# Kernel tuning notes

Measured on AMD Instinct MI355X. Metric: run time of the kernel, lower is better.

## Reference

```python
import jax, jax.numpy as jnp
import numpy as np

B, S, D, A = 8, 4096, 128, 128


def _pos_encoding(seq_len, dim):
    # sin/cos positional encoding, same construction as the torch buffer
    pos = np.arange(seq_len, dtype=np.float32)[:, None]
    div = np.exp(np.arange(0, dim, 2, dtype=np.float32) * (-np.log(10000.0) / dim))
    pe = np.zeros((seq_len, dim), dtype=np.float32)
    pe[:, 0::2] = np.sin(pos * div)
    pe[:, 1::2] = np.cos(pos * div)
    return jnp.asarray(pe)


def setup_inputs() -> dict:
    key = jax.random.key(0)
    ks = jax.random.split(key, 7)
    sc = 1.0 / np.sqrt(D)
    return {
        "x": jax.random.normal(ks[0], (B, S, D), dtype=jnp.float32),
        "Wq": jax.random.normal(ks[1], (D, A), dtype=jnp.float32) * sc,
        "bq": jnp.zeros((A,), dtype=jnp.float32),
        "Wk": jax.random.normal(ks[2], (D, A), dtype=jnp.float32) * sc,
        "bk": jnp.zeros((A,), dtype=jnp.float32),
        "Wv": jax.random.normal(ks[3], (D, A), dtype=jnp.float32) * sc,
        "bv": jnp.zeros((A,), dtype=jnp.float32),
    }


def reference(x, Wq, bq, Wk, bk, Wv, bv):
    b, s, d = x.shape
    pe = _pos_encoding(s, d)  # [S, D]
    xp = x + pe[None]  # broadcast add of positional encoding
    q = xp @ Wq + bq  # [B, S, A]
    k = xp @ Wk + bk
    v = xp @ Wv + bv
    scale = 1.0 / jnp.sqrt(jnp.asarray(Wq.shape[1], dtype=jnp.float32))
    scores = jnp.einsum("bsa,bta->bst", q, k) * scale  # [B, S, S]
    weights = jax.nn.softmax(scores, axis=-1)
    out = jnp.einsum("bst,bta->bsa", weights, v)  # [B, S, A]
    return out
```

## Files before the change

kernel.cpp:

```cpp
#include <hip/hip_runtime.h>

#define BB 8
#define SS 4096
#define DD 128

typedef __attribute__((ext_vector_type(8))) short v8s;
typedef __attribute__((ext_vector_type(4))) short v4s;
typedef __attribute__((ext_vector_type(4))) float v4f;
typedef __attribute__((ext_vector_type(16))) float v16f;

__device__ __forceinline__ unsigned short f2bf(float f) {
    unsigned int u = __float_as_uint(f);
    u += 0x7fffu + ((u >> 16) & 1u);
    return (unsigned short)(u >> 16);
}
__device__ __forceinline__ unsigned int pk_bf16(float a, float b) {
    unsigned int ua = __float_as_uint(a) + 0x8000u;
    unsigned int ub = __float_as_uint(b) + 0x8000u;
    return __builtin_amdgcn_perm(ub, ua, 0x07060302u);
}

#if !defined(__HIP_DEVICE_COMPILE__)
#define MFMA16(a, b, c) (c)
#define MFMA32(a, b, c) (c)
#else
#define MFMA16(a, b, c) __builtin_amdgcn_mfma_f32_16x16x32_bf16((a), (b), (c), 0, 0, 0)
#define MFMA32(a, b, c) __builtin_amdgcn_mfma_f32_32x32x16_bf16((a), (b), (c), 0, 0, 0)
#endif

#if !defined(__HIP_DEVICE_COMPILE__)
#define EXP2F(x) exp2f(x)
#elif __has_builtin(__builtin_amdgcn_exp2f)
#define EXP2F(x) __builtin_amdgcn_exp2f(x)
#else
#define EXP2F(x) exp2f(x)
#endif

#define QSCALE 0.12751743f
#define FIXM 24.0f

__global__ __launch_bounds__(256) void prep_kernel(
    const float* __restrict__ Wq, const float* __restrict__ Wk,
    const float* __restrict__ Wv, unsigned short* __restrict__ Wt,
    float* __restrict__ pe)
{
    int bid = blockIdx.x;
    int tid = threadIdx.x;
    if (bid < 192) {
        int id = bid * 256 + tid;
        int w = id >> 14;
        int n = (id >> 7) & 127;
        int k = id & 127;
        const float* W = (w == 0) ? Wq : (w == 1) ? Wk : Wv;
        Wt[id] = f2bf(W[k * 128 + n]);
    } else {
        int id = (bid - 192) * 256 + tid;
        int s = id >> 5;
        int d0 = (id & 31) * 4;
        v4f r;
#pragma unroll
        for (int j = 0; j < 4; j += 2) {
            float freq = __expf((float)(d0 + j) * -0.07195578415606394f);
            float arg = (float)s * freq;
            r[j] = __sinf(arg);
            r[j + 1] = __cosf(arg);
        }
        *(v4f*)(pe + (size_t)s * DD + d0) = r;
    }
}

__global__ __launch_bounds__(256, 3) void proj_kernel(
    const float* __restrict__ x, const float* __restrict__ pe,
    const unsigned short* __restrict__ Wt,
    const float* __restrict__ bq, const float* __restrict__ bk,
    const float* __restrict__ bv,
    unsigned short* __restrict__ qo, unsigned short* __restrict__ ko,
    unsigned short* __restrict__ vo)
{
    __shared__ __attribute__((aligned(16))) unsigned short w_lds[128 * 136];
    __shared__ __attribute__((aligned(16))) unsigned short o_lds[9216];

    const int tid = threadIdx.x;
    const int wave = tid >> 6;
    const int lane = tid & 63;
    const int quad = lane >> 4;
    const int l15 = lane & 15;
    const int bid = blockIdx.x;
    const int mat = bid % 3;
    const int rbase = (bid / 3) * 64;

    const unsigned short* Wp = Wt + (mat << 14);
#pragma unroll
    for (int it = 0; it < 8; ++it) {
        int id = it * 256 + tid;
        int n = id >> 4, c8 = id & 15;
        *(v8s*)(w_lds + n * 136 + c8 * 8) = *(const v8s*)(Wp + n * 128 + c8 * 8);
    }

    const int flatrow = rbase + wave * 16 + l15;
    const int srow = flatrow & 4095;
    v8s af[4];
#pragma unroll
    for (int kc = 0; kc < 4; ++kc) {
        const int kbase = kc * 32 + quad * 8;
        const v4f* xp = (const v4f*)(x + (size_t)flatrow * DD + kbase);
        const v4f* pp = (const v4f*)(pe + (size_t)srow * DD + kbase);
        v4f x0 = xp[0], x1 = xp[1], p0 = pp[0], p1 = pp[1];
        v8s a;
#pragma unroll
        for (int j = 0; j < 4; ++j) a[j] = (short)f2bf(x0[j] + p0[j]);
#pragma unroll
        for (int j = 0; j < 4; ++j) a[4 + j] = (short)f2bf(x1[j] + p1[j]);
        af[kc] = a;
    }

    const float* bias = (mat == 0) ? bq : (mat == 1) ? bk : bv;
    __syncthreads();

#pragma unroll
    for (int nb = 0; nb < 8; ++nb) {
        const int col = nb * 16 + l15;
        v4f acc = {0.f, 0.f, 0.f, 0.f};
#pragma unroll
        for (int kc = 0; kc < 4; ++kc) {
            v8s bf = *(const v8s*)(w_lds + col * 136 + kc * 32 + quad * 8);
            acc = MFMA16(af[kc], bf, acc);
        }
        float bval = bias[col];
#pragma unroll
        for (int reg = 0; reg < 4; ++reg) {
            int lr = wave * 16 + quad * 4 + reg;
            float val = acc[reg] + bval;
            if (mat == 0) {
                o_lds[lr * 136 + col] = f2bf(val * QSCALE);
            } else if (mat == 1) {
                o_lds[lr * 136 + col] = f2bf(val);
            } else {
                o_lds[col * 72 + lr] = f2bf(val);
            }
        }
    }
    __syncthreads();

    if (mat <= 1) {
        unsigned short* outp = (mat == 0) ? qo : ko;
#pragma unroll
        for (int it = 0; it < 4; ++it) {
            int id = it * 256 + tid;
            int r = id >> 4, c8 = id & 15;
            *(v8s*)(outp + (size_t)(rbase + r) * DD + c8 * 8) =
                *(const v8s*)(o_lds + r * 136 + c8 * 8);
        }
    } else {
        const int b0 = rbase >> 12, s0 = rbase & 4095;
#pragma unroll
        for (int it = 0; it < 4; ++it) {
            int id = it * 256 + tid;
            int a = id >> 3, c = id & 7;
            *(v8s*)(vo + ((size_t)(b0 * 128 + a)) * SS + s0 + c * 8) =
                *(const v8s*)(o_lds + a * 72 + c * 8);
        }
    }
}

#define KT 32
#define HKEYS 2048
#define NT (HKEYS / KT)
__global__ __launch_bounds__(512, 2) void flash_kernel(
    const unsigned short* __restrict__ qg,
    const unsigned short* __restrict__ kg,
    const unsigned short* __restrict__ vg,
    float* __restrict__ out)
{
    __shared__ __attribute__((aligned(16))) unsigned short k_lds[2][2][4096];
    __shared__ __attribute__((aligned(16))) unsigned short v_lds[2][2][4096];
    __shared__ float xl[128];

    const int tid = threadIdx.x;
    const int wave = tid >> 6;
    const int lane = tid & 63;
    const int hi = lane >> 5;
    const int l31 = lane & 31;
    const int half = tid >> 8;
    const int qs = wave & 3;
    const int bid = blockIdx.x;
    const int b = bid & 7;
    const int qt = bid >> 3;
    const int qbase = qt * 128;

    const size_t qrow = (size_t)(b * SS + qbase + qs * 32 + l31) * DD;
    v8s qf[8];
#pragma unroll
    for (int kc = 0; kc < 8; ++kc)
        qf[kc] = *(const v8s*)(qg + qrow + kc * 16 + hi * 8);

    v16f o[4];
#pragma unroll
    for (int fg = 0; fg < 4; ++fg)
#pragma unroll
        for (int r = 0; r < 16; ++r) o[fg][r] = 0.f;
    v16f lacc;
#pragma unroll
    for (int r = 0; r < 16; ++r) lacc[r] = 0.f;

    v8s ones;
#pragma unroll
    for (int j = 0; j < 8; ++j) ones[j] = (short)0x3F80;

    const unsigned short* kb = kg + (size_t)b * SS * DD + (size_t)half * HKEYS * DD;
    const unsigned short* vb = vg + (size_t)b * DD * SS + half * HKEYS;

    const int tid2 = tid & 255;
    const int kr_r = tid2 >> 4, kr_c = tid2 & 15;
    const int va = tid2 >> 2, vc8 = tid2 & 3;
    v8s kr[2], vr[2];

    auto load_tile = [&](int t) {
        const unsigned short* kp = kb + (size_t)t * KT * DD;
        const unsigned short* vp = vb + t * KT;
#pragma unroll
        for (int it = 0; it < 2; ++it) {
            kr[it] = *(const v8s*)(kp + (size_t)(kr_r + it * 16) * DD + kr_c * 8);
            vr[it] = *(const v8s*)(vp + (size_t)(va + it * 64) * SS + vc8 * 8);
        }
    };
    auto store_tile = [&](int p) {
#pragma unroll
        for (int it = 0; it < 2; ++it) {
            int r = kr_r + it * 16;
            *(v8s*)(&k_lds[half][p][r * 128 + ((kr_c ^ (r & 7)) << 3)]) = kr[it];
            int a = va + it * 64;
            v4s lo = {vr[it][0], vr[it][1], vr[it][2], vr[it][3]};
            v4s hv = {vr[it][4], vr[it][5], vr[it][6], vr[it][7]};
            int cc = vc8 >> 1, h = vc8 & 1;
            int sw = (a & 3) ^ ((a >> 2) & 1);
            *(v4s*)(&v_lds[half][p][a * 32 + (((cc ^ sw) << 3) + h * 4)]) = lo;
            *(v4s*)(&v_lds[half][p][a * 32 + ((((cc + 2) ^ sw) << 3) + h * 4)]) = hv;
        }
    };
    auto compute = [&](int p) {
        v16f s;
#pragma unroll
        for (int r = 0; r < 16; ++r) s[r] = -FIXM;
#pragma unroll
        for (int kc = 0; kc < 8; ++kc) {
            v8s af = *(const v8s*)(&k_lds[half][p][l31 * 128 +
                                   (((kc * 2 + hi) ^ (l31 & 7)) << 3)]);
            s = MFMA32(af, qf[kc], s);
        }
        float e[16];
#pragma unroll
        for (int r = 0; r < 16; ++r) e[r] = EXP2F(s[r]);
        union { v8s v[2]; unsigned int u[8]; } P;
#pragma unroll
        for (int g = 0; g < 2; ++g)
#pragma unroll
            for (int m = 0; m < 4; ++m)
                P.u[g * 4 + m] = pk_bf16(e[2 * m + 8 * g], e[2 * m + 8 * g + 1]);
#pragma unroll
        for (int g = 0; g < 2; ++g) {
            lacc = MFMA32(P.v[g], ones, lacc);
#pragma unroll
            for (int fg = 0; fg < 4; ++fg) {
                int row = fg * 32 + l31;
                int sw = (row & 3) ^ ((row >> 2) & 1);
                v8s bf = *(const v8s*)(&v_lds[half][p][row * 32 +
                                       (((2 * hi + g) ^ sw) << 3)]);
                o[fg] = MFMA32(P.v[g], bf, o[fg]);
            }
        }
    };

    load_tile(0);
    store_tile(0);
    load_tile(1);
    __syncthreads();
#pragma unroll 1
    for (int kt = 0; kt < NT; kt += 2) {
        store_tile(1);
        if (kt + 2 < NT) load_tile(kt + 2);
        compute(0);
        __syncthreads();
        if (kt + 2 < NT) {
            store_tile(0);
            if (kt + 3 < NT) load_tile(kt + 3);
        }
        compute(1);
        __syncthreads();
    }

    float* kf = (float*)&k_lds[0][0][0];
    float* vf = (float*)&v_lds[0][0][0];
    float* xch = (qs < 2) ? (kf + qs * 4096) : (vf + (qs - 2) * 4096);

    if (half == 1) {
#pragma unroll
        for (int fg = 0; fg < 4; ++fg) {
            v4f* base = (v4f*)(xch + fg * 1024 + lane * 16);
#pragma unroll
            for (int c = 0; c < 4; ++c) {
                v4f t = {o[fg][c * 4 + 0], o[fg][c * 4 + 1],
                         o[fg][c * 4 + 2], o[fg][c * 4 + 3]};
                base[c ^ (lane & 3)] = t;
            }
        }
        if (l31 == 0) {
#pragma unroll
            for (int r = 0; r < 16; ++r) {
                int qr = (r & 3) + 8 * (r >> 2) + 4 * hi;
                xl[qs * 32 + qr] = lacc[r];
            }
        }
    }
    __syncthreads();
    if (half == 0) {
#pragma unroll
        for (int fg = 0; fg < 4; ++fg) {
            const v4f* base = (const v4f*)(xch + fg * 1024 + lane * 16);
#pragma unroll
            for (int c = 0; c < 4; ++c) {
                v4f t = base[c ^ (lane & 3)];
#pragma unroll
                for (int j = 0; j < 4; ++j) o[fg][c * 4 + j] += t[j];
            }
        }
        float ir[16];
#pragma unroll
        for (int r = 0; r < 16; ++r) {
            int qr = (r & 3) + 8 * (r >> 2) + 4 * hi;
            ir[r] = 1.0f / (lacc[r] + xl[qs * 32 + qr]);
        }
#pragma unroll
        for (int fg = 0; fg < 4; ++fg)
#pragma unroll
            for (int r = 0; r < 16; ++r) {
                int qr = (r & 3) + 8 * (r >> 2) + 4 * hi;
                out[(size_t)(b * SS + qbase + qs * 32 + qr) * DD + fg * 32 + l31] =
                    o[fg][r] * ir[r];
            }
    }
}

extern "C" void kernel_launch(void* const* d_in, const int* in_sizes, int n_in,
                              void* d_out, int out_size, void* d_ws, size_t ws_size,
                              hipStream_t stream)
{
    const float* x  = (const float*)d_in[0];
    const float* Wq = (const float*)d_in[1];
    const float* bq = (const float*)d_in[2];
    const float* Wk = (const float*)d_in[3];
    const float* bk = (const float*)d_in[4];
    const float* Wv = (const float*)d_in[5];
    const float* bv = (const float*)d_in[6];
    float* out = (float*)d_out;

    unsigned short* Wt = (unsigned short*)d_ws;
    unsigned short* q  = Wt + 49152;
    unsigned short* k  = q + (size_t)BB * SS * DD;
    unsigned short* vT = k + (size_t)BB * SS * DD;
    float* pe = (float*)(vT + (size_t)BB * SS * DD);

    hipLaunchKernelGGL(prep_kernel, dim3(704), dim3(256), 0, stream,
                       Wq, Wk, Wv, Wt, pe);
    hipLaunchKernelGGL(proj_kernel, dim3(BB * SS / 64 * 3), dim3(256), 0, stream,
                       x, pe, Wt, bq, bk, bv, q, k, vT);
    hipLaunchKernelGGL(flash_kernel, dim3(BB * SS / 128), dim3(512), 0, stream,
                       q, k, vT, out);
}
```

Measured before the change: 179.0 us.

## Restructure flash kernel: direct global-to-LDS loads, 4-way key split, 64-row waves

The attention kernel now stages K/V tiles with global_load_lds straight into LDS instead of going through registers, synchronised with explicit vmcnt/lgkmcnt waits and raw barriers. Keys are split four ways across wave pairs, with each wave handling 64 query rows (two MFMA accumulator sets), so each K/V LDS fragment read is reused twice. Row sums are now taken with VALU adds instead of an MFMA against a ones vector, and the fixed -24 offset is dropped. The cost is a three-step LDS reduction of partial outputs and higher register pressure. The V layout in the prep kernel is permuted to match the new LDS swizzle.

```diff
diff --git a/kernel.cpp b/kernel.cpp
--- a/kernel.cpp
+++ b/kernel.cpp
@@ -5,7 +5,6 @@
 #define DD 128
 
 typedef __attribute__((ext_vector_type(8))) short v8s;
-typedef __attribute__((ext_vector_type(4))) short v4s;
 typedef __attribute__((ext_vector_type(4))) float v4f;
 typedef __attribute__((ext_vector_type(16))) float v16f;
 
@@ -23,9 +22,26 @@
 #if !defined(__HIP_DEVICE_COMPILE__)
 #define MFMA16(a, b, c) (c)
 #define MFMA32(a, b, c) (c)
+#define GLDS16(g, l)
+#define WAITVM(n)
+#define WAITLGKM()
+#define BAR()
 #else
 #define MFMA16(a, b, c) __builtin_amdgcn_mfma_f32_16x16x32_bf16((a), (b), (c), 0, 0, 0)
 #define MFMA32(a, b, c) __builtin_amdgcn_mfma_f32_32x32x16_bf16((a), (b), (c), 0, 0, 0)
+#define GLDS16(g, l)                                                         \
+    __builtin_amdgcn_global_load_lds(                                        \
+        (const __attribute__((address_space(1))) unsigned int*)(g),          \
+        (__attribute__((address_space(3))) unsigned int*)(l), 16, 0, 0)
+#define WAITVM(n) asm volatile("s_waitcnt vmcnt(" #n ")" ::: "memory")
+#define WAITLGKM() asm volatile("s_waitcnt lgkmcnt(0)" ::: "memory")
+#define BAR()                                                                \
+    do {                                                                     \
+        asm volatile("" ::: "memory");                                       \
+        __builtin_amdgcn_s_barrier();                                        \
+        __builtin_amdgcn_sched_barrier(0);                                   \
+        asm volatile("" ::: "memory");                                       \
+    } while (0)
 #endif
 
 #if !defined(__HIP_DEVICE_COMPILE__)
@@ -37,7 +53,6 @@
 #endif
 
 #define QSCALE 0.12751743f
-#define FIXM 24.0f
 
 __global__ __launch_bounds__(256) void prep_kernel(
     const float* __restrict__ Wq, const float* __restrict__ Wk,
@@ -115,6 +130,7 @@
     }
 
     const float* bias = (mat == 0) ? bq : (mat == 1) ? bk : bv;
+    const int quadp = ((quad & 1) << 1) | (quad >> 1);
     __syncthreads();
 
 #pragma unroll
@@ -129,14 +145,16 @@
         float bval = bias[col];
 #pragma unroll
         for (int reg = 0; reg < 4; ++reg) {
-            int lr = wave * 16 + quad * 4 + reg;
             float val = acc[reg] + bval;
             if (mat == 0) {
+                int lr = wave * 16 + quad * 4 + reg;
                 o_lds[lr * 136 + col] = f2bf(val * QSCALE);
             } else if (mat == 1) {
+                int lr = wave * 16 + quad * 4 + reg;
                 o_lds[lr * 136 + col] = f2bf(val);
             } else {
-                o_lds[col * 72 + lr] = f2bf(val);
+                int plr = wave * 16 + quadp * 4 + reg;
+                o_lds[col * 72 + plr] = f2bf(val);
             }
         }
     }
@@ -164,180 +182,203 @@
 }
 
 #define KT 32
-#define HKEYS 2048
-#define NT (HKEYS / KT)
+#define QKEYS 1024
+#define NT2 (QKEYS / KT)
 __global__ __launch_bounds__(512, 2) void flash_kernel(
-    const unsigned short* __restrict__ qg,
-    const unsigned short* __restrict__ kg,
-    const unsigned short* __restrict__ vg,
-    float* __restrict__ out)
+    const unsigned short* __restrict__ qp,
+    const unsigned short* __restrict__ kp,
+    const unsigned short* __restrict__ vp,
+    float* __restrict__ outp)
 {
-    __shared__ __attribute__((aligned(16))) unsigned short k_lds[2][2][4096];
-    __shared__ __attribute__((aligned(16))) unsigned short v_lds[2][2][4096];
-    __shared__ float xl[128];
+    __shared__ __attribute__((aligned(16))) unsigned short k_lds[4][2][4096];
+    __shared__ __attribute__((aligned(16))) unsigned short v_lds[4][2][4096];
+    __shared__ float xl[8][64];
 
     const int tid = threadIdx.x;
     const int wave = tid >> 6;
     const int lane = tid & 63;
     const int hi = lane >> 5;
     const int l31 = lane & 31;
-    const int half = tid >> 8;
-    const int qs = wave & 3;
+    const int qtr = wave >> 1;
+    const int w = wave & 1;
+    const int qs = wave & 1;
     const int bid = blockIdx.x;
     const int b = bid & 7;
     const int qt = bid >> 3;
     const int qbase = qt * 128;
 
-    const size_t qrow = (size_t)(b * SS + qbase + qs * 32 + l31) * DD;
-    v8s qf[8];
-#pragma unroll
-    for (int kc = 0; kc < 8; ++kc)
-        qf[kc] = *(const v8s*)(qg + qrow + kc * 16 + hi * 8);
-
-    v16f o[4];
+    const size_t qrow0 = (size_t)(b * SS + qbase + qs * 64 + l31) * DD;
+    v8s qf0[8], qf1[8];
+#pragma unroll
+    for (int kc = 0; kc < 8; ++kc) {
+        qf0[kc] = *(const v8s*)(qp + qrow0 + kc * 16 + hi * 8);
+        qf1[kc] = *(const v8s*)(qp + qrow0 + (size_t)32 * DD + kc * 16 + hi * 8);
+    }
+
+    v16f o0[4], o1[4];
 #pragma unroll
     for (int fg = 0; fg < 4; ++fg)
 #pragma unroll
-        for (int r = 0; r < 16; ++r) o[fg][r] = 0.f;
-    v16f lacc;
-#pragma unroll
-    for (int r = 0; r < 16; ++r) lacc[r] = 0.f;
-
-    v8s ones;
-#pragma unroll
-    for (int j = 0; j < 8; ++j) ones[j] = (short)0x3F80;
-
-    const unsigned short* kb = kg + (size_t)b * SS * DD + (size_t)half * HKEYS * DD;
-    const unsigned short* vb = vg + (size_t)b * DD * SS + half * HKEYS;
-
-    const int tid2 = tid & 255;
-    const int kr_r = tid2 >> 4, kr_c = tid2 & 15;
-    const int va = tid2 >> 2, vc8 = tid2 & 3;
-    v8s kr[2], vr[2];
-
-    auto load_tile = [&](int t) {
-        const unsigned short* kp = kb + (size_t)t * KT * DD;
-        const unsigned short* vp = vb + t * KT;
-#pragma unroll
-        for (int it = 0; it < 2; ++it) {
-            kr[it] = *(const v8s*)(kp + (size_t)(kr_r + it * 16) * DD + kr_c * 8);
-            vr[it] = *(const v8s*)(vp + (size_t)(va + it * 64) * SS + vc8 * 8);
-        }
+        for (int r = 0; r < 16; ++r) { o0[fg][r] = 0.f; o1[fg][r] = 0.f; }
+    float lp0 = 0.f, lp1 = 0.f;
+
+    const int koff = qtr * 16384 + l31 * 256 + ((hi << 4) ^ ((l31 & 7) << 4));
+    const int hx3 = (hi << 4) ^ ((l31 & 3) << 4);
+    const int vaddr0 = qtr * 16384 + l31 * 64 + hx3;
+    const int vaddr1 = qtr * 16384 + l31 * 64 + (hx3 ^ 32);
+
+    const int krw = lane >> 4, ksl = lane & 15;
+    const int e_sh = krw * 128 + ((ksl ^ krw) << 3);
+    const unsigned short* kq =
+        kp + ((size_t)(b * SS) + qtr * QKEYS) * DD + w * 2048;
+    const unsigned short* kp0_ = kq + e_sh;
+    const unsigned short* kp4_ = kq + (e_sh ^ 32);
+    const int vrw = lane >> 2, vsl = lane & 3;
+    const int e_v = vrw * 4096 + ((vsl ^ (vrw & 3)) << 3);
+    const unsigned short* vq =
+        vp + (size_t)b * DD * SS + qtr * QKEYS + (size_t)w * 262144 + e_v;
+
+    auto stage = [&](int p, int t) {
+        unsigned short* kd = &k_lds[qtr][p][w * 2048];
+        unsigned short* vd = &v_lds[qtr][p][w * 2048];
+        const unsigned short* ks0 = kp0_ + (size_t)t * 4096;
+        const unsigned short* ks4 = kp4_ + (size_t)t * 4096;
+        const unsigned short* vs = vq + (size_t)t * 32;
+        GLDS16(ks0, kd);
+        GLDS16(ks4 + 512, kd + 512);
+        GLDS16(ks0 + 1024, kd + 1024);
+        GLDS16(ks4 + 1536, kd + 1536);
+        GLDS16(vs, vd);
+        GLDS16(vs + 65536, vd + 512);
+        GLDS16(vs + 131072, vd + 1024);
+        GLDS16(vs + 196608, vd + 1536);
     };
-    auto store_tile = [&](int p) {
-#pragma unroll
-        for (int it = 0; it < 2; ++it) {
-            int r = kr_r + it * 16;
-            *(v8s*)(&k_lds[half][p][r * 128 + ((kr_c ^ (r & 7)) << 3)]) = kr[it];
-            int a = va + it * 64;
-            v4s lo = {vr[it][0], vr[it][1], vr[it][2], vr[it][3]};
-            v4s hv = {vr[it][4], vr[it][5], vr[it][6], vr[it][7]};
-            int cc = vc8 >> 1, h = vc8 & 1;
-            int sw = (a & 3) ^ ((a >> 2) & 1);
-            *(v4s*)(&v_lds[half][p][a * 32 + (((cc ^ sw) << 3) + h * 4)]) = lo;
-            *(v4s*)(&v_lds[half][p][a * 32 + ((((cc + 2) ^ sw) << 3) + h * 4)]) = hv;
+
+    auto compute = [&](int p) {
+        v16f s0, s1;
+#pragma unroll
+        for (int r = 0; r < 16; ++r) { s0[r] = 0.f; s1[r] = 0.f; }
+#pragma unroll
+        for (int kc = 0; kc < 8; ++kc) {
+            v8s af = *(const v8s*)((const char*)k_lds +
+                                   ((koff ^ (kc << 5)) + p * 8192));
+            s0 = MFMA32(af, qf0[kc], s0);
+            s1 = MFMA32(af, qf1[kc], s1);
+        }
+        union PU { v8s v[2]; unsigned int u[8]; } P0, P1;
+        float e[16];
+#pragma unroll
+        for (int r = 0; r < 16; ++r) e[r] = EXP2F(s0[r]);
+        lp0 += (((e[0] + e[1]) + (e[2] + e[3])) + ((e[4] + e[5]) + (e[6] + e[7]))) +
+               (((e[8] + e[9]) + (e[10] + e[11])) + ((e[12] + e[13]) + (e[14] + e[15])));
+#pragma unroll
+        for (int g = 0; g < 2; ++g)
+#pragma unroll
+            for (int m = 0; m < 4; ++m)
+                P0.u[g * 4 + m] = pk_bf16(e[2 * m + 8 * g], e[2 * m + 8 * g + 1]);
+#pragma unroll
+        for (int r = 0; r < 16; ++r) e[r] = EXP2F(s1[r]);
+        lp1 += (((e[0] + e[1]) + (e[2] + e[3])) + ((e[4] + e[5]) + (e[6] + e[7]))) +
+               (((e[8] + e[9]) + (e[10] + e[11])) + ((e[12] + e[13]) + (e[14] + e[15])));
+#pragma unroll
+        for (int g = 0; g < 2; ++g)
+#pragma unroll
+            for (int m = 0; m < 4; ++m)
+                P1.u[g * 4 + m] = pk_bf16(e[2 * m + 8 * g], e[2 * m + 8 * g + 1]);
+#pragma unroll
+        for (int g = 0; g < 2; ++g) {
+            const int va = g ? vaddr1 : vaddr0;
+#pragma unroll
+            for (int fg = 0; fg < 4; ++fg) {
+                v8s bf = *(const v8s*)((const char*)v_lds +
+                                       (va + fg * 2048 + p * 8192));
+                o0[fg] = MFMA32(P0.v[g], bf, o0[fg]);
+                o1[fg] = MFMA32(P1.v[g], bf, o1[fg]);
+            }
         }
     };
-    auto compute = [&](int p) {
-        v16f s;
-#pragma unroll
-        for (int r = 0; r < 16; ++r) s[r] = -FIXM;
-#pragma unroll
-        for (int kc = 0; kc < 8; ++kc) {
-            v8s af = *(const v8s*)(&k_lds[half][p][l31 * 128 +
-                                   (((kc * 2 + hi) ^ (l31 & 7)) << 3)]);
-            s = MFMA32(af, qf[kc], s);
-        }
-        float e[16];
-#pragma unroll
-        for (int r = 0; r < 16; ++r) e[r] = EXP2F(s[r]);
-        union { v8s v[2]; unsigned int u[8]; } P;
-#pragma unroll
-        for (int g = 0; g < 2; ++g)
-#pragma unroll
-            for (int m = 0; m < 4; ++m)
-                P.u[g * 4 + m] = pk_bf16(e[2 * m + 8 * g], e[2 * m + 8 * g + 1]);
-#pragma unroll
-        for (int g = 0; g < 2; ++g) {
-            lacc = MFMA32(P.v[g], ones, lacc);
-#pragma unroll
-            for (int fg = 0; fg < 4; ++fg) {
-                int row = fg * 32 + l31;
-                int sw = (row & 3) ^ ((row >> 2) & 1);
-                v8s bf = *(const v8s*)(&v_lds[half][p][row * 32 +
-                                       (((2 * hi + g) ^ sw) << 3)]);
-                o[fg] = MFMA32(P.v[g], bf, o[fg]);
-            }
-        }
-    };
-
-    load_tile(0);
-    store_tile(0);
-    load_tile(1);
-    __syncthreads();
+
+    stage(0, 0);
 #pragma unroll 1
-    for (int kt = 0; kt < NT; kt += 2) {
-        store_tile(1);
-        if (kt + 2 < NT) load_tile(kt + 2);
+    for (int t = 0; t < NT2; t += 2) {
+        stage(1, t + 1);
+        WAITVM(8);
+        BAR();
         compute(0);
-        __syncthreads();
-        if (kt + 2 < NT) {
-            store_tile(0);
-            if (kt + 3 < NT) load_tile(kt + 3);
-        }
+        WAITLGKM();
+        BAR();
+        if (t + 2 < NT2) {
+            stage(0, t + 2);
+            WAITVM(8);
+        } else {
+            WAITVM(0);
+        }
+        BAR();
         compute(1);
-        __syncthreads();
-    }
+        WAITLGKM();
+        BAR();
+    }
+
+    lp0 += __shfl_xor(lp0, 32);
+    lp1 += __shfl_xor(lp1, 32);
+    if (hi == 0) { xl[wave][l31] = lp0; xl[wave][32 + l31] = lp1; }
 
     float* kf = (float*)&k_lds[0][0][0];
     float* vf = (float*)&v_lds[0][0][0];
-    float* xch = (qs < 2) ? (kf + qs * 4096) : (vf + (qs - 2) * 4096);
-
-    if (half == 1) {
-#pragma unroll
-        for (int fg = 0; fg < 4; ++fg) {
-            v4f* base = (v4f*)(xch + fg * 1024 + lane * 16);
+
+    auto putO = [&](float* base) {
+#pragma unroll
+        for (int qgf = 0; qgf < 8; ++qgf) {
+            const v16f& ov = (qgf < 4) ? o0[qgf] : o1[qgf - 4];
 #pragma unroll
             for (int c = 0; c < 4; ++c) {
-                v4f t = {o[fg][c * 4 + 0], o[fg][c * 4 + 1],
-                         o[fg][c * 4 + 2], o[fg][c * 4 + 3]};
-                base[c ^ (lane & 3)] = t;
-            }
-        }
-        if (l31 == 0) {
+                v4f tv = {ov[c * 4 + 0], ov[c * 4 + 1], ov[c * 4 + 2], ov[c * 4 + 3]};
+                *(v4f*)(base + (qgf * 4 + c) * 256 + lane * 4) = tv;
+            }
+        }
+    };
+    auto addO = [&](const float* base) {
+#pragma unroll
+        for (int qgf = 0; qgf < 8; ++qgf) {
+            v16f& ov = (qgf < 4) ? o0[qgf] : o1[qgf - 4];
+#pragma unroll
+            for (int c = 0; c < 4; ++c) {
+                v4f tv = *(const v4f*)(base + (qgf * 4 + c) * 256 + lane * 4);
+#pragma unroll
+                for (int j = 0; j < 4; ++j) ov[c * 4 + j] += tv[j];
+            }
+        }
+    };
+
+    if (qtr & 1) putO(((qtr == 1) ? kf : vf) + qs * 8192);
+    __syncthreads();
+    if (!(qtr & 1)) addO(((qtr == 0) ? kf : vf) + qs * 8192);
+    __syncthreads();
+    if (qtr == 2) putO(kf + qs * 8192);
+    __syncthreads();
+    if (qtr == 0) {
+        addO(kf + qs * 8192);
+#pragma unroll
+        for (int qg2 = 0; qg2 < 2; ++qg2) {
+            float ir[16];
 #pragma unroll
             for (int r = 0; r < 16; ++r) {
-                int qr = (r & 3) + 8 * (r >> 2) + 4 * hi;
-                xl[qs * 32 + qr] = lacc[r];
-            }
-        }
-    }
-    __syncthreads();
-    if (half == 0) {
-#pragma unroll
-        for (int fg = 0; fg < 4; ++fg) {
-            const v4f* base = (const v4f*)(xch + fg * 1024 + lane * 16);
-#pragma unroll
-            for (int c = 0; c < 4; ++c) {
-                v4f t = base[c ^ (lane & 3)];
-#pragma unroll
-                for (int j = 0; j < 4; ++j) o[fg][c * 4 + j] += t[j];
-            }
-        }
-        float ir[16];
-#pragma unroll
-        for (int r = 0; r < 16; ++r) {
-            int qr = (r & 3) + 8 * (r >> 2) + 4 * hi;
-            ir[r] = 1.0f / (lacc[r] + xl[qs * 32 + qr]);
-        }
-#pragma unroll
-        for (int fg = 0; fg < 4; ++fg)
-#pragma unroll
-            for (int r = 0; r < 16; ++r) {
-                int qr = (r & 3) + 8 * (r >> 2) + 4 * hi;
-                out[(size_t)(b * SS + qbase + qs * 32 + qr) * DD + fg * 32 + l31] =
-                    o[fg][r] * ir[r];
-            }
+                int qrow = (r & 3) + 8 * (r >> 2) + 4 * hi;
+                float ls = xl[0 + qs][qg2 * 32 + qrow] + xl[2 + qs][qg2 * 32 + qrow] +
+                           xl[4 + qs][qg2 * 32 + qrow] + xl[6 + qs][qg2 * 32 + qrow];
+                ir[r] = 1.0f / ls;
+            }
+#pragma unroll
+            for (int fg = 0; fg < 4; ++fg) {
+                const v16f& ov = qg2 ? o1[fg] : o0[fg];
+#pragma unroll
+                for (int r = 0; r < 16; ++r) {
+                    int qrow = (r & 3) + 8 * (r >> 2) + 4 * hi;
+                    outp[(size_t)(b * SS + qbase + qs * 64 + qg2 * 32 + qrow) * DD +
+                         fg * 32 + l31] = ov[r] * ir[r];
+                }
+            }
+        }
     }
 }
 
```

Result: slower. 202.4 us (+13.1%).
